# Performance work log

Hardware: AMD Instinct MI355X
Metric: run time of the kernel (lower is better)

Reference implementation:

```python
import jax, jax.numpy as jnp
import numpy as np

E = 32      # particle_embed_dim = q/k/v head out dim
G = 2       # nof_net_types (conv groups)
NEG_SLOPE = 0.01


def _glin(x, w, b, groups):
    """Grouped 1x1 conv on (M, C, 1, 1) == grouped linear.
    x: (M, Cin), w: (Cout, Cin//groups), b: (Cout,)."""
    M = x.shape[0]
    Cout = w.shape[0]
    xg = x.reshape(M, groups, -1)                 # (M, G, Cin/G)
    wg = w.reshape(groups, Cout // groups, -1)    # (G, Cout/G, Cin/G)
    y = jnp.einsum('mgi,goi->mgo', xg, wg).reshape(M, Cout)
    return y + b


def setup_inputs() -> dict:
    key = jax.random.key(0)
    ks = jax.random.split(key, 9)
    B, N = 32, 1024
    s = 0.05
    return {
        'x_e':   jax.random.normal(ks[0], (B, N, G * E), dtype=jnp.float32),
        'w_qkv': jax.random.normal(ks[1], (3 * G * E, E), dtype=jnp.float32) * s,
        'b_qkv': jax.random.normal(ks[2], (3 * G * E,), dtype=jnp.float32) * s,
        'w_h1':  jax.random.normal(ks[3], (G * E, 2 * E), dtype=jnp.float32) * s,
        'b_h1':  jax.random.normal(ks[4], (G * E,), dtype=jnp.float32) * s,
        'w_h10': jax.random.normal(ks[5], (G * E, E), dtype=jnp.float32) * s,
        'b_h10': jax.random.normal(ks[6], (G * E,), dtype=jnp.float32) * s,
        'w_h11': jax.random.normal(ks[7], (G * E, E), dtype=jnp.float32) * s,
        'b_h11': jax.random.normal(ks[8], (G * E,), dtype=jnp.float32) * s,
    }


def reference(x_e, w_qkv, b_qkv, w_h1, b_h1, w_h10, b_h10, w_h11, b_h11):
    B, N, D = x_e.shape                      # D = G*E = 64
    act = lambda z: jnp.where(z >= 0, z, NEG_SLOPE * z)

    # grouped 1x1-conv QKV projection
    qkv = _glin(x_e.reshape(B * N, D), w_qkv, b_qkv, G)        # (B*N, 3*G*E)
    qkv = qkv.reshape(B, N, G, 3, E).transpose(0, 2, 3, 1, 4)  # (B, G, 3, N, E)
    q, k, v = qkv[:, :, 0], qkv[:, :, 1], qkv[:, :, 2]         # each (B, G, N, E)

    # NOTE: module divides k by sqrt(E) and logits by sqrt(E) again -> 1/E total
    scale = 1.0 / E
    ip = jnp.einsum('bgne,bgme->bgnm', q, k) * scale           # (B, G, N, N)
    sip = jax.nn.softmax(ip, axis=-1)
    attn = jnp.einsum('bgnm,bgme->bgne', sip, v)               # (B, G, N, E)

    # concat pre-attention v with attention output, regroup per-particle
    x_xe = jnp.concatenate([v, attn], axis=3)                  # (B, G, N, 2E)
    x_xe = x_xe.transpose(0, 2, 1, 3).reshape(B * N, G * 2 * E)  # (B*N, 128)

    h = act(_glin(x_xe, w_h1, b_h1, G))
    h = act(_glin(h, w_h10, b_h10, G))
    h = act(_glin(h, w_h11, b_h11, G))
    return h.reshape(B * N, G * E, 1, 1)
```

## Files before the change

kernel.cpp:

```cpp
#include <hip/hip_runtime.h>

#define B_ 32
#define N_ 1024
#define G_ 2
#define E_ 32
#define M_ (B_*N_)
#define NEG 0.01f
#define QT 128
#define KT 128
#define QSC (1.4426950408889634f/32.0f)

using half8  = __attribute__((ext_vector_type(8))) _Float16;
using half4  = __attribute__((ext_vector_type(4))) _Float16;
using floatx4 = __attribute__((ext_vector_type(4))) float;

#if defined(__has_builtin)
#if __has_builtin(__builtin_amdgcn_exp2f)
#define EXP2(x) __builtin_amdgcn_exp2f(x)
#endif
#endif
#ifndef EXP2
#define EXP2(x) exp2f(x)
#endif

__global__ __launch_bounds__(256) void qkv_kernel(
    const float* __restrict__ x, const float* __restrict__ w, const float* __restrict__ bias,
    _Float16* __restrict__ Qh, _Float16* __restrict__ Kh,
    _Float16* __restrict__ Vh, _Float16* __restrict__ Vth)
{
    __shared__ _Float16 wsh[192*36];
    __shared__ float bsh[192];
    int t = threadIdx.x;
    for (int idx = t; idx < 192*32; idx += 256) {
        int r = idx >> 5, c = idx & 31;
        wsh[r*36 + c] = (_Float16)w[idx];
    }
    if (t < 192) bsh[t] = bias[t];
    __syncthreads();

    int lane = t & 63, wv = t >> 6;
    int L15 = lane & 15, quad = lane >> 4;
    int row0 = blockIdx.x*64 + wv*16;
    int b = row0 >> 10, nn0 = row0 & 1023;

    half4 ax[2][2];
    #pragma unroll
    for (int g2 = 0; g2 < 2; g2++)
        #pragma unroll
        for (int kt = 0; kt < 2; kt++) {
            float4 f = *(const float4*)(x + (size_t)(row0+L15)*64 + g2*32 + kt*16 + quad*4);
            half4 h = { (_Float16)f.x, (_Float16)f.y, (_Float16)f.z, (_Float16)f.w };
            ax[g2][kt] = h;
        }

    floatx4 acc[12];
    #pragma unroll
    for (int i = 0; i < 12; i++) acc[i] = (floatx4){0.f,0.f,0.f,0.f};

    #pragma unroll
    for (int g2 = 0; g2 < 2; g2++)
        #pragma unroll
        for (int nt = 0; nt < 6; nt++)
            #pragma unroll
            for (int kt = 0; kt < 2; kt++) {
                half4 bw = *(const half4*)&wsh[(g2*96+nt*16+L15)*36 + kt*16 + quad*4];
                acc[g2*6+nt] = __builtin_amdgcn_mfma_f32_16x16x16f16(ax[g2][kt], bw, acc[g2*6+nt], 0,0,0);
            }

    #pragma unroll
    for (int g2 = 0; g2 < 2; g2++) {
        size_t bg = (size_t)(b*2 + g2);
        #pragma unroll
        for (int nt = 0; nt < 6; nt++) {
            float bia = bsh[g2*96 + nt*16 + L15];
            floatx4 a4 = acc[g2*6+nt];
            int e = (nt & 1)*16 + L15;
            int kind = nt >> 1;
            if (kind == 0) {
                #pragma unroll
                for (int r = 0; r < 4; r++) {
                    int nn = nn0 + quad*4 + r;
                    Qh[(bg*N_ + nn)*32 + e] = (_Float16)((a4[r] + bia)*QSC);
                }
            } else if (kind == 1) {
                #pragma unroll
                for (int r = 0; r < 4; r++) {
                    int nn = nn0 + quad*4 + r;
                    Kh[(bg*N_ + nn)*32 + e] = (_Float16)(a4[r] + bia);
                }
            } else {
                half4 vv;
                #pragma unroll
                for (int r = 0; r < 4; r++) {
                    int nn = nn0 + quad*4 + r;
                    float vval = a4[r] + bia;
                    Vh[(bg*N_ + nn)*32 + e] = (_Float16)vval;
                    vv[r] = (_Float16)vval;
                }
                *(half4*)(Vth + (bg*32 + e)*N_ + nn0 + quad*4) = vv;
            }
        }
    }
}

struct __align__(16) SmemU {
    union {
        struct { _Float16 Kst[128*40]; _Float16 Vtst[32*136]; } a;
        _Float16 xs[128*72];
    } u;
    float linv[128];
    float bl1[32], bl10[32], bl11[32];
};

__global__ __launch_bounds__(256) void attn_mlp_kernel(
    const _Float16* __restrict__ Qh, const _Float16* __restrict__ Kh,
    const _Float16* __restrict__ Vh, const _Float16* __restrict__ Vth,
    const float* __restrict__ w_h1,  const float* __restrict__ b_h1,
    const float* __restrict__ w_h10, const float* __restrict__ b_h10,
    const float* __restrict__ w_h11, const float* __restrict__ b_h11,
    float* __restrict__ out)
{
    __shared__ SmemU sm;
    int t = threadIdx.x;
    int bg = blockIdx.x >> 3;
    int qtile = blockIdx.x & 7;
    int b = bg >> 1, g = bg & 1;
    int qbase = qtile * QT;
    size_t bgN = (size_t)bg * N_;

    if (t < 32) {
        sm.bl1[t]  = b_h1[g*32+t];
        sm.bl10[t] = b_h10[g*32+t];
        sm.bl11[t] = b_h11[g*32+t];
    }

    int lane = t & 63;
    int w    = t >> 6;
    int L15  = lane & 15;
    int quad = lane >> 4;
    int q0w  = qbase + w*32;

    half8 bq0 = *(const half8*)(Qh + (bgN + q0w +      L15)*32 + quad*8);
    half8 bq1 = *(const half8*)(Qh + (bgN + q0w + 16 + L15)*32 + quad*8);

    floatx4 o00 = {0.f,0.f,0.f,0.f}, o01 = o00, o10 = o00, o11 = o00;
    float lsum0 = 0.f, lsum1 = 0.f;

    for (int kt = 0; kt < N_/KT; kt++) {
        __syncthreads();
        #pragma unroll
        for (int it = 0; it < 2; it++) {
            int idx = t + it*256;
            int row = idx >> 2, c = idx & 3;
            half8 kv = *(const half8*)(Kh + (bgN + (size_t)kt*KT + row)*32 + c*8);
            *(half8*)&sm.u.a.Kst[row*40 + c*8] = kv;
        }
        #pragma unroll
        for (int it = 0; it < 2; it++) {
            int idx = t + it*256;
            int ee = idx >> 4, c = idx & 15;
            half8 vv = *(const half8*)(Vth + (size_t)bg*(32*N_) + (size_t)ee*N_ + kt*KT + c*8);
            *(half8*)&sm.u.a.Vtst[ee*136 + c*8] = vv;
        }
        __syncthreads();

        #pragma unroll
        for (int mt = 0; mt < 8; mt++) {
            half8 ak = *(const half8*)&sm.u.a.Kst[(mt*16 + L15)*40 + quad*8];
            floatx4 z = {0.f,0.f,0.f,0.f};
            floatx4 s0 = __builtin_amdgcn_mfma_f32_16x16x32_f16(ak, bq0, z, 0, 0, 0);
            floatx4 s1 = __builtin_amdgcn_mfma_f32_16x16x32_f16(ak, bq1, z, 0, 0, 0);
            float p00 = EXP2(s0.x), p01 = EXP2(s0.y), p02 = EXP2(s0.z), p03 = EXP2(s0.w);
            float p10 = EXP2(s1.x), p11 = EXP2(s1.y), p12 = EXP2(s1.z), p13 = EXP2(s1.w);
            lsum0 += (p00+p01)+(p02+p03);
            lsum1 += (p10+p11)+(p12+p13);
            half4 a0 = { (_Float16)p00, (_Float16)p01, (_Float16)p02, (_Float16)p03 };
            half4 a1 = { (_Float16)p10, (_Float16)p11, (_Float16)p12, (_Float16)p13 };
            half4 bv0 = *(const half4*)&sm.u.a.Vtst[      L15*136 + mt*16 + quad*4];
            half4 bv1 = *(const half4*)&sm.u.a.Vtst[(16+L15)*136 + mt*16 + quad*4];
            o00 = __builtin_amdgcn_mfma_f32_16x16x16f16(a0, bv0, o00, 0, 0, 0);
            o01 = __builtin_amdgcn_mfma_f32_16x16x16f16(a0, bv1, o01, 0, 0, 0);
            o10 = __builtin_amdgcn_mfma_f32_16x16x16f16(a1, bv0, o10, 0, 0, 0);
            o11 = __builtin_amdgcn_mfma_f32_16x16x16f16(a1, bv1, o11, 0, 0, 0);
        }
    }

    lsum0 += __shfl_xor(lsum0, 16, 64); lsum0 += __shfl_xor(lsum0, 32, 64);
    lsum1 += __shfl_xor(lsum1, 16, 64); lsum1 += __shfl_xor(lsum1, 32, 64);
    if (quad == 0) {
        sm.linv[w*32 +      L15] = 1.0f / lsum0;
        sm.linv[w*32 + 16 + L15] = 1.0f / lsum1;
    }
    __syncthreads();

    for (int idx = t; idx < 512; idx += 256) {
        int row = idx >> 2, c = idx & 3;
        half8 vv = *(const half8*)(Vh + (bgN + qbase + row)*32 + c*8);
        *(half8*)&sm.u.xs[row*72 + c*8] = vv;
    }
    {
        const floatx4* ofr[2][2] = { {&o00,&o01}, {&o10,&o11} };
        #pragma unroll
        for (int nt = 0; nt < 2; nt++) {
            float4 li = *(const float4*)&sm.linv[w*32 + nt*16 + quad*4];
            #pragma unroll
            for (int et = 0; et < 2; et++) {
                floatx4 ov = *ofr[nt][et];
                sm.u.xs[(w*32+nt*16+quad*4+0)*72 + 32 + et*16 + L15] = (_Float16)(ov[0]*li.x);
                sm.u.xs[(w*32+nt*16+quad*4+1)*72 + 32 + et*16 + L15] = (_Float16)(ov[1]*li.y);
                sm.u.xs[(w*32+nt*16+quad*4+2)*72 + 32 + et*16 + L15] = (_Float16)(ov[2]*li.z);
                sm.u.xs[(w*32+nt*16+quad*4+3)*72 + 32 + et*16 + L15] = (_Float16)(ov[3]*li.w);
            }
        }
    }
    __syncthreads();

    half4 a1f[2][4], a2f[2][2], a3f[2][2];
    #pragma unroll
    for (int mt = 0; mt < 2; mt++) {
        #pragma unroll
        for (int kt = 0; kt < 4; kt++) {
            float4 f = *(const float4*)(w_h1 + (size_t)(g*32+mt*16+L15)*64 + kt*16 + quad*4);
            half4 h = { (_Float16)f.x, (_Float16)f.y, (_Float16)f.z, (_Float16)f.w };
            a1f[mt][kt] = h;
        }
        #pragma unroll
        for (int kt = 0; kt < 2; kt++) {
            float4 f = *(const float4*)(w_h10 + (size_t)(g*32+mt*16+L15)*32 + kt*16 + quad*4);
            half4 h = { (_Float16)f.x, (_Float16)f.y, (_Float16)f.z, (_Float16)f.w };
            a2f[mt][kt] = h;
            float4 f2 = *(const float4*)(w_h11 + (size_t)(g*32+mt*16+L15)*32 + kt*16 + quad*4);
            half4 h2 = { (_Float16)f2.x, (_Float16)f2.y, (_Float16)f2.z, (_Float16)f2.w };
            a3f[mt][kt] = h2;
        }
    }

    floatx4 d1[2][2];
    #pragma unroll
    for (int mt = 0; mt < 2; mt++)
        #pragma unroll
        for (int nt = 0; nt < 2; nt++) d1[mt][nt] = (floatx4){0.f,0.f,0.f,0.f};
    #pragma unroll
    for (int nt = 0; nt < 2; nt++)
        #pragma unroll
        for (int kt = 0; kt < 4; kt++) {
            half4 b1 = *(const half4*)&sm.u.xs[(w*32+nt*16+L15)*72 + kt*16 + quad*4];
            d1[0][nt] = __builtin_amdgcn_mfma_f32_16x16x16f16(a1f[0][kt], b1, d1[0][nt], 0,0,0);
            d1[1][nt] = __builtin_amdgcn_mfma_f32_16x16x16f16(a1f[1][kt], b1, d1[1][nt], 0,0,0);
        }
    half4 h1b[2][2];
    #pragma unroll
    for (int mt = 0; mt < 2; mt++) {
        float4 bb = *(const float4*)&sm.bl1[mt*16 + quad*4];
        #pragma unroll
        for (int nt = 0; nt < 2; nt++) {
            float v0 = d1[mt][nt][0] + bb.x; v0 = (v0>=0.f)?v0:NEG*v0;
            float v1 = d1[mt][nt][1] + bb.y; v1 = (v1>=0.f)?v1:NEG*v1;
            float v2 = d1[mt][nt][2] + bb.z; v2 = (v2>=0.f)?v2:NEG*v2;
            float v3 = d1[mt][nt][3] + bb.w; v3 = (v3>=0.f)?v3:NEG*v3;
            half4 h = { (_Float16)v0, (_Float16)v1, (_Float16)v2, (_Float16)v3 };
            h1b[mt][nt] = h;
        }
    }
    floatx4 d2[2][2];
    #pragma unroll
    for (int mt = 0; mt < 2; mt++)
        #pragma unroll
        for (int nt = 0; nt < 2; nt++) d2[mt][nt] = (floatx4){0.f,0.f,0.f,0.f};
    #pragma unroll
    for (int mt = 0; mt < 2; mt++)
        #pragma unroll
        for (int nt = 0; nt < 2; nt++)
            #pragma unroll
            for (int kt = 0; kt < 2; kt++)
                d2[mt][nt] = __builtin_amdgcn_mfma_f32_16x16x16f16(a2f[mt][kt], h1b[kt][nt], d2[mt][nt], 0,0,0);
    half4 h2b[2][2];
    #pragma unroll
    for (int mt = 0; mt < 2; mt++) {
        float4 bb = *(const float4*)&sm.bl10[mt*16 + quad*4];
        #pragma unroll
        for (int nt = 0; nt < 2; nt++) {
            float v0 = d2[mt][nt][0] + bb.x; v0 = (v0>=0.f)?v0:NEG*v0;
            float v1 = d2[mt][nt][1] + bb.y; v1 = (v1>=0.f)?v1:NEG*v1;
            float v2 = d2[mt][nt][2] + bb.z; v2 = (v2>=0.f)?v2:NEG*v2;
            float v3 = d2[mt][nt][3] + bb.w; v3 = (v3>=0.f)?v3:NEG*v3;
            half4 h = { (_Float16)v0, (_Float16)v1, (_Float16)v2, (_Float16)v3 };
            h2b[mt][nt] = h;
        }
    }
    floatx4 d3[2][2];
    #pragma unroll
    for (int mt = 0; mt < 2; mt++)
        #pragma unroll
        for (int nt = 0; nt < 2; nt++) d3[mt][nt] = (floatx4){0.f,0.f,0.f,0.f};
    #pragma unroll
    for (int mt = 0; mt < 2; mt++)
        #pragma unroll
        for (int nt = 0; nt < 2; nt++)
            #pragma unroll
            for (int kt = 0; kt < 2; kt++)
                d3[mt][nt] = __builtin_amdgcn_mfma_f32_16x16x16f16(a3f[mt][kt], h2b[kt][nt], d3[mt][nt], 0,0,0);
    #pragma unroll
    for (int mt = 0; mt < 2; mt++) {
        float4 bb = *(const float4*)&sm.bl11[mt*16 + quad*4];
        #pragma unroll
        for (int nt = 0; nt < 2; nt++) {
            size_t rowbase = ((size_t)b*N_ + qbase + w*32 + nt*16 + L15)*64 + g*32 + mt*16 + quad*4;
            float v0 = d3[mt][nt][0] + bb.x; out[rowbase+0] = (v0>=0.f)?v0:NEG*v0;
            float v1 = d3[mt][nt][1] + bb.y; out[rowbase+1] = (v1>=0.f)?v1:NEG*v1;
            float v2 = d3[mt][nt][2] + bb.z; out[rowbase+2] = (v2>=0.f)?v2:NEG*v2;
            float v3 = d3[mt][nt][3] + bb.w; out[rowbase+3] = (v3>=0.f)?v3:NEG*v3;
        }
    }
}

extern "C" void kernel_launch(void* const* d_in, const int* in_sizes, int n_in,
                              void* d_out, int out_size, void* d_ws, size_t ws_size,
                              hipStream_t stream) {
    const float* x_e   = (const float*)d_in[0];
    const float* w_qkv = (const float*)d_in[1];
    const float* b_qkv = (const float*)d_in[2];
    const float* w_h1  = (const float*)d_in[3];
    const float* b_h1  = (const float*)d_in[4];
    const float* w_h10 = (const float*)d_in[5];
    const float* b_h10 = (const float*)d_in[6];
    const float* w_h11 = (const float*)d_in[7];
    const float* b_h11 = (const float*)d_in[8];
    float* out = (float*)d_out;

    const size_t qkv_elems = (size_t)B_*G_*N_*E_;
    _Float16* Qh  = (_Float16*)d_ws;
    _Float16* Kh  = Qh + qkv_elems;
    _Float16* Vh  = Kh + qkv_elems;
    _Float16* Vth = Vh + qkv_elems;

    hipLaunchKernelGGL(qkv_kernel, dim3(M_/64), dim3(256), 0, stream,
                       x_e, w_qkv, b_qkv, Qh, Kh, Vh, Vth);
    hipLaunchKernelGGL(attn_mlp_kernel, dim3(B_*G_*(N_/QT)), dim3(256), 0, stream,
                       Qh, Kh, Vh, Vth, w_h1, b_h1, w_h10, b_h10, w_h11, b_h11, out);
}
```

Measured before the change: 105.7 us.

## Halve attention query tile, stage QKV outputs in LDS for coalesced stores

The attention kernel now handles 64 queries per block with 16 per wave, doubling the grid to 1024 blocks and declaring 4 blocks per CU in the launch bounds for better occupancy. The QKV projection now writes Q, K, V and the transposed V into shared-memory tiles and then stores them to global memory as coalesced half8 vectors, replacing scattered 2-byte stores. The final MLP output is written as float4. In exchange, each block re-reads the full K and V^T for only 64 queries, doubling K/V traffic from L2, and the QKV kernel now uses more LDS.

After: 110.6 us. 1.05x slower.

```diff
diff --git a/kernel.cpp b/kernel.cpp
--- a/kernel.cpp
+++ b/kernel.cpp
@@ -6,7 +6,7 @@
 #define E_ 32
 #define M_ (B_*N_)
 #define NEG 0.01f
-#define QT 128
+#define QT 64
 #define KT 128
 #define QSC (1.4426950408889634f/32.0f)
 
@@ -30,6 +30,8 @@
 {
     __shared__ _Float16 wsh[192*36];
     __shared__ float bsh[192];
+    __shared__ _Float16 sQ[64*72], sK[64*72], sV[64*72];
+    __shared__ _Float16 vT[64*72];
     int t = threadIdx.x;
     for (int idx = t; idx < 192*32; idx += 256) {
         int r = idx >> 5, c = idx & 31;
@@ -41,7 +43,7 @@
     int lane = t & 63, wv = t >> 6;
     int L15 = lane & 15, quad = lane >> 4;
     int row0 = blockIdx.x*64 + wv*16;
-    int b = row0 >> 10, nn0 = row0 & 1023;
+    int b = row0 >> 10, nn0g = (blockIdx.x*64) & 1023;
 
     half4 ax[2][2];
     #pragma unroll
@@ -69,50 +71,61 @@
 
     #pragma unroll
     for (int g2 = 0; g2 < 2; g2++) {
-        size_t bg = (size_t)(b*2 + g2);
         #pragma unroll
         for (int nt = 0; nt < 6; nt++) {
             float bia = bsh[g2*96 + nt*16 + L15];
             floatx4 a4 = acc[g2*6+nt];
             int e = (nt & 1)*16 + L15;
             int kind = nt >> 1;
+            int rbase = wv*16 + quad*4;
             if (kind == 0) {
                 #pragma unroll
-                for (int r = 0; r < 4; r++) {
-                    int nn = nn0 + quad*4 + r;
-                    Qh[(bg*N_ + nn)*32 + e] = (_Float16)((a4[r] + bia)*QSC);
-                }
+                for (int r = 0; r < 4; r++)
+                    sQ[(rbase+r)*72 + g2*32 + e] = (_Float16)((a4[r] + bia)*QSC);
             } else if (kind == 1) {
                 #pragma unroll
-                for (int r = 0; r < 4; r++) {
-                    int nn = nn0 + quad*4 + r;
-                    Kh[(bg*N_ + nn)*32 + e] = (_Float16)(a4[r] + bia);
-                }
+                for (int r = 0; r < 4; r++)
+                    sK[(rbase+r)*72 + g2*32 + e] = (_Float16)(a4[r] + bia);
             } else {
                 half4 vv;
                 #pragma unroll
                 for (int r = 0; r < 4; r++) {
-                    int nn = nn0 + quad*4 + r;
                     float vval = a4[r] + bia;
-                    Vh[(bg*N_ + nn)*32 + e] = (_Float16)vval;
+                    sV[(rbase+r)*72 + g2*32 + e] = (_Float16)vval;
                     vv[r] = (_Float16)vval;
                 }
-                *(half4*)(Vth + (bg*32 + e)*N_ + nn0 + quad*4) = vv;
+                *(half4*)&vT[(g2*32+e)*72 + rbase] = vv;
             }
         }
+    }
+    __syncthreads();
+
+    int r = t >> 2, c8 = t & 3;
+    #pragma unroll
+    for (int g2 = 0; g2 < 2; g2++) {
+        size_t gbase = (((size_t)(b*2+g2))*N_ + nn0g + r)*32 + c8*8;
+        *(half8*)(Qh + gbase) = *(const half8*)&sQ[r*72 + g2*32 + c8*8];
+        *(half8*)(Kh + gbase) = *(const half8*)&sK[r*72 + g2*32 + c8*8];
+        *(half8*)(Vh + gbase) = *(const half8*)&sV[r*72 + g2*32 + c8*8];
+    }
+    #pragma unroll
+    for (int it = 0; it < 2; it++) {
+        int idx = t + it*256;
+        int ge = idx >> 3, c = idx & 7;
+        *(half8*)(Vth + ((size_t)(b*2)*32 + ge)*N_ + nn0g + c*8) = *(const half8*)&vT[ge*72 + c*8];
     }
 }
 
 struct __align__(16) SmemU {
     union {
         struct { _Float16 Kst[128*40]; _Float16 Vtst[32*136]; } a;
-        _Float16 xs[128*72];
+        _Float16 xs[64*72];
     } u;
-    float linv[128];
+    float linv[64];
     float bl1[32], bl10[32], bl11[32];
 };
 
-__global__ __launch_bounds__(256) void attn_mlp_kernel(
+__global__ __launch_bounds__(256, 4) void attn_mlp_kernel(
     const _Float16* __restrict__ Qh, const _Float16* __restrict__ Kh,
     const _Float16* __restrict__ Vh, const _Float16* __restrict__ Vth,
     const float* __restrict__ w_h1,  const float* __restrict__ b_h1,
@@ -122,8 +135,8 @@
 {
     __shared__ SmemU sm;
     int t = threadIdx.x;
-    int bg = blockIdx.x >> 3;
-    int qtile = blockIdx.x & 7;
+    int bg = blockIdx.x >> 4;
+    int qtile = blockIdx.x & 15;
     int b = bg >> 1, g = bg & 1;
     int qbase = qtile * QT;
     size_t bgN = (size_t)bg * N_;
@@ -138,13 +151,12 @@
     int w    = t >> 6;
     int L15  = lane & 15;
     int quad = lane >> 4;
-    int q0w  = qbase + w*32;
-
-    half8 bq0 = *(const half8*)(Qh + (bgN + q0w +      L15)*32 + quad*8);
-    half8 bq1 = *(const half8*)(Qh + (bgN + q0w + 16 + L15)*32 + quad*8);
-
-    floatx4 o00 = {0.f,0.f,0.f,0.f}, o01 = o00, o10 = o00, o11 = o00;
-    float lsum0 = 0.f, lsum1 = 0.f;
+    int q0w  = qbase + w*16;
+
+    half8 bq = *(const half8*)(Qh + (bgN + q0w + L15)*32 + quad*8);
+
+    floatx4 o0 = {0.f,0.f,0.f,0.f}, o1 = o0;
+    float lsum = 0.f;
 
     for (int kt = 0; kt < N_/KT; kt++) {
         __syncthreads();
@@ -168,49 +180,36 @@
         for (int mt = 0; mt < 8; mt++) {
             half8 ak = *(const half8*)&sm.u.a.Kst[(mt*16 + L15)*40 + quad*8];
             floatx4 z = {0.f,0.f,0.f,0.f};
-            floatx4 s0 = __builtin_amdgcn_mfma_f32_16x16x32_f16(ak, bq0, z, 0, 0, 0);
-            floatx4 s1 = __builtin_amdgcn_mfma_f32_16x16x32_f16(ak, bq1, z, 0, 0, 0);
-            float p00 = EXP2(s0.x), p01 = EXP2(s0.y), p02 = EXP2(s0.z), p03 = EXP2(s0.w);
-            float p10 = EXP2(s1.x), p11 = EXP2(s1.y), p12 = EXP2(s1.z), p13 = EXP2(s1.w);
-            lsum0 += (p00+p01)+(p02+p03);
-            lsum1 += (p10+p11)+(p12+p13);
-            half4 a0 = { (_Float16)p00, (_Float16)p01, (_Float16)p02, (_Float16)p03 };
-            half4 a1 = { (_Float16)p10, (_Float16)p11, (_Float16)p12, (_Float16)p13 };
+            floatx4 s = __builtin_amdgcn_mfma_f32_16x16x32_f16(ak, bq, z, 0, 0, 0);
+            float p0 = EXP2(s.x), p1 = EXP2(s.y), p2 = EXP2(s.z), p3 = EXP2(s.w);
+            lsum += (p0+p1)+(p2+p3);
+            half4 a0 = { (_Float16)p0, (_Float16)p1, (_Float16)p2, (_Float16)p3 };
             half4 bv0 = *(const half4*)&sm.u.a.Vtst[      L15*136 + mt*16 + quad*4];
             half4 bv1 = *(const half4*)&sm.u.a.Vtst[(16+L15)*136 + mt*16 + quad*4];
-            o00 = __builtin_amdgcn_mfma_f32_16x16x16f16(a0, bv0, o00, 0, 0, 0);
-            o01 = __builtin_amdgcn_mfma_f32_16x16x16f16(a0, bv1, o01, 0, 0, 0);
-            o10 = __builtin_amdgcn_mfma_f32_16x16x16f16(a1, bv0, o10, 0, 0, 0);
-            o11 = __builtin_amdgcn_mfma_f32_16x16x16f16(a1, bv1, o11, 0, 0, 0);
-        }
-    }
-
-    lsum0 += __shfl_xor(lsum0, 16, 64); lsum0 += __shfl_xor(lsum0, 32, 64);
-    lsum1 += __shfl_xor(lsum1, 16, 64); lsum1 += __shfl_xor(lsum1, 32, 64);
-    if (quad == 0) {
-        sm.linv[w*32 +      L15] = 1.0f / lsum0;
-        sm.linv[w*32 + 16 + L15] = 1.0f / lsum1;
-    }
+            o0 = __builtin_amdgcn_mfma_f32_16x16x16f16(a0, bv0, o0, 0, 0, 0);
+            o1 = __builtin_amdgcn_mfma_f32_16x16x16f16(a0, bv1, o1, 0, 0, 0);
+        }
+    }
+
+    lsum += __shfl_xor(lsum, 16, 64); lsum += __shfl_xor(lsum, 32, 64);
+    if (quad == 0) sm.linv[w*16 + L15] = 1.0f / lsum;
     __syncthreads();
 
-    for (int idx = t; idx < 512; idx += 256) {
-        int row = idx >> 2, c = idx & 3;
+    {
+        int row = t >> 2, c = t & 3;
         half8 vv = *(const half8*)(Vh + (bgN + qbase + row)*32 + c*8);
         *(half8*)&sm.u.xs[row*72 + c*8] = vv;
     }
     {
-        const floatx4* ofr[2][2] = { {&o00,&o01}, {&o10,&o11} };
-        #pragma unroll
-        for (int nt = 0; nt < 2; nt++) {
-            float4 li = *(const float4*)&sm.linv[w*32 + nt*16 + quad*4];
-            #pragma unroll
-            for (int et = 0; et < 2; et++) {
-                floatx4 ov = *ofr[nt][et];
-                sm.u.xs[(w*32+nt*16+quad*4+0)*72 + 32 + et*16 + L15] = (_Float16)(ov[0]*li.x);
-                sm.u.xs[(w*32+nt*16+quad*4+1)*72 + 32 + et*16 + L15] = (_Float16)(ov[1]*li.y);
-                sm.u.xs[(w*32+nt*16+quad*4+2)*72 + 32 + et*16 + L15] = (_Float16)(ov[2]*li.z);
-                sm.u.xs[(w*32+nt*16+quad*4+3)*72 + 32 + et*16 + L15] = (_Float16)(ov[3]*li.w);
-            }
+        float4 li = *(const float4*)&sm.linv[w*16 + quad*4];
+        const floatx4* ofr[2] = { &o0, &o1 };
+        #pragma unroll
+        for (int et = 0; et < 2; et++) {
+            floatx4 ov = *ofr[et];
+            sm.u.xs[(w*16+quad*4+0)*72 + 32 + et*16 + L15] = (_Float16)(ov[0]*li.x);
+            sm.u.xs[(w*16+quad*4+1)*72 + 32 + et*16 + L15] = (_Float16)(ov[1]*li.y);
+            sm.u.xs[(w*16+quad*4+2)*72 + 32 + et*16 + L15] = (_Float16)(ov[2]*li.z);
+            sm.u.xs[(w*16+quad*4+3)*72 + 32 + et*16 + L15] = (_Float16)(ov[3]*li.w);
         }
     }
     __syncthreads();
@@ -235,82 +234,56 @@
         }
     }
 
-    floatx4 d1[2][2];
-    #pragma unroll
-    for (int mt = 0; mt < 2; mt++)
-        #pragma unroll
-        for (int nt = 0; nt < 2; nt++) d1[mt][nt] = (floatx4){0.f,0.f,0.f,0.f};
-    #pragma unroll
-    for (int nt = 0; nt < 2; nt++)
-        #pragma unroll
-        for (int kt = 0; kt < 4; kt++) {
-            half4 b1 = *(const half4*)&sm.u.xs[(w*32+nt*16+L15)*72 + kt*16 + quad*4];
-            d1[0][nt] = __builtin_amdgcn_mfma_f32_16x16x16f16(a1f[0][kt], b1, d1[0][nt], 0,0,0);
-            d1[1][nt] = __builtin_amdgcn_mfma_f32_16x16x16f16(a1f[1][kt], b1, d1[1][nt], 0,0,0);
-        }
-    half4 h1b[2][2];
+    floatx4 d1[2] = { {0.f,0.f,0.f,0.f}, {0.f,0.f,0.f,0.f} };
+    #pragma unroll
+    for (int kt = 0; kt < 4; kt++) {
+        half4 b1 = *(const half4*)&sm.u.xs[(w*16+L15)*72 + kt*16 + quad*4];
+        d1[0] = __builtin_amdgcn_mfma_f32_16x16x16f16(a1f[0][kt], b1, d1[0], 0,0,0);
+        d1[1] = __builtin_amdgcn_mfma_f32_16x16x16f16(a1f[1][kt], b1, d1[1], 0,0,0);
+    }
+    half4 h1b[2];
     #pragma unroll
     for (int mt = 0; mt < 2; mt++) {
         float4 bb = *(const float4*)&sm.bl1[mt*16 + quad*4];
-        #pragma unroll
-        for (int nt = 0; nt < 2; nt++) {
-            float v0 = d1[mt][nt][0] + bb.x; v0 = (v0>=0.f)?v0:NEG*v0;
-            float v1 = d1[mt][nt][1] + bb.y; v1 = (v1>=0.f)?v1:NEG*v1;
-            float v2 = d1[mt][nt][2] + bb.z; v2 = (v2>=0.f)?v2:NEG*v2;
-            float v3 = d1[mt][nt][3] + bb.w; v3 = (v3>=0.f)?v3:NEG*v3;
-            half4 h = { (_Float16)v0, (_Float16)v1, (_Float16)v2, (_Float16)v3 };
-            h1b[mt][nt] = h;
-        }
-    }
-    floatx4 d2[2][2];
+        float v0 = d1[mt][0] + bb.x; v0 = (v0>=0.f)?v0:NEG*v0;
+        float v1 = d1[mt][1] + bb.y; v1 = (v1>=0.f)?v1:NEG*v1;
+        float v2 = d1[mt][2] + bb.z; v2 = (v2>=0.f)?v2:NEG*v2;
+        float v3 = d1[mt][3] + bb.w; v3 = (v3>=0.f)?v3:NEG*v3;
+        half4 h = { (_Float16)v0, (_Float16)v1, (_Float16)v2, (_Float16)v3 };
+        h1b[mt] = h;
+    }
+    floatx4 d2[2] = { {0.f,0.f,0.f,0.f}, {0.f,0.f,0.f,0.f} };
     #pragma unroll
     for (int mt = 0; mt < 2; mt++)
         #pragma unroll
-        for (int nt = 0; nt < 2; nt++) d2[mt][nt] = (floatx4){0.f,0.f,0.f,0.f};
-    #pragma unroll
-    for (int mt = 0; mt < 2; mt++)
-        #pragma unroll
-        for (int nt = 0; nt < 2; nt++)
-            #pragma unroll
-            for (int kt = 0; kt < 2; kt++)
-                d2[mt][nt] = __builtin_amdgcn_mfma_f32_16x16x16f16(a2f[mt][kt], h1b[kt][nt], d2[mt][nt], 0,0,0);
-    half4 h2b[2][2];
+        for (int kt = 0; kt < 2; kt++)
+            d2[mt] = __builtin_amdgcn_mfma_f32_16x16x16f16(a2f[mt][kt], h1b[kt], d2[mt], 0,0,0);
+    half4 h2b[2];
     #pragma unroll
     for (int mt = 0; mt < 2; mt++) {
         float4 bb = *(const float4*)&sm.bl10[mt*16 + quad*4];
-        #pragma unroll
-        for (int nt = 0; nt < 2; nt++) {
-            float v0 = d2[mt][nt][0] + bb.x; v0 = (v0>=0.f)?v0:NEG*v0;
-            float v1 = d2[mt][nt][1] + bb.y; v1 = (v1>=0.f)?v1:NEG*v1;
-            float v2 = d2[mt][nt][2] + bb.z; v2 = (v2>=0.f)?v2:NEG*v2;
-            float v3 = d2[mt][nt][3] + bb.w; v3 = (v3>=0.f)?v3:NEG*v3;
-            half4 h = { (_Float16)v0, (_Float16)v1, (_Float16)v2, (_Float16)v3 };
-            h2b[mt][nt] = h;
-        }
-    }
-    floatx4 d3[2][2];
+        float v0 = d2[mt][0] + bb.x; v0 = (v0>=0.f)?v0:NEG*v0;
+        float v1 = d2[mt][1] + bb.y; v1 = (v1>=0.f)?v1:NEG*v1;
+        float v2 = d2[mt][2] + bb.z; v2 = (v2>=0.f)?v2:NEG*v2;
+        float v3 = d2[mt][3] + bb.w; v3 = (v3>=0.f)?v3:NEG*v3;
+        half4 h = { (_Float16)v0, (_Float16)v1, (_Float16)v2, (_Float16)v3 };
+        h2b[mt] = h;
+    }
+    floatx4 d3[2] = { {0.f,0.f,0.f,0.f}, {0.f,0.f,0.f,0.f} };
     #pragma unroll
     for (int mt = 0; mt < 2; mt++)
         #pragma unroll
-        for (int nt = 0; nt < 2; nt++) d3[mt][nt] = (floatx4){0.f,0.f,0.f,0.f};
-    #pragma unroll
-    for (int mt = 0; mt < 2; mt++)
-        #pragma unroll
-        for (int nt = 0; nt < 2; nt++)
-            #pragma unroll
-            for (int kt = 0; kt < 2; kt++)
-                d3[mt][nt] = __builtin_amdgcn_mfma_f32_16x16x16f16(a3f[mt][kt], h2b[kt][nt], d3[mt][nt], 0,0,0);
+        for (int kt = 0; kt < 2; kt++)
+            d3[mt] = __builtin_amdgcn_mfma_f32_16x16x16f16(a3f[mt][kt], h2b[kt], d3[mt], 0,0,0);
     #pragma unroll
     for (int mt = 0; mt < 2; mt++) {
         float4 bb = *(const float4*)&sm.bl11[mt*16 + quad*4];
-        #pragma unroll
-        for (int nt = 0; nt < 2; nt++) {
-            size_t rowbase = ((size_t)b*N_ + qbase + w*32 + nt*16 + L15)*64 + g*32 + mt*16 + quad*4;
-            float v0 = d3[mt][nt][0] + bb.x; out[rowbase+0] = (v0>=0.f)?v0:NEG*v0;
-            float v1 = d3[mt][nt][1] + bb.y; out[rowbase+1] = (v1>=0.f)?v1:NEG*v1;
-            float v2 = d3[mt][nt][2] + bb.z; out[rowbase+2] = (v2>=0.f)?v2:NEG*v2;
-            float v3 = d3[mt][nt][3] + bb.w; out[rowbase+3] = (v3>=0.f)?v3:NEG*v3;
-        }
+        float4 ov;
+        ov.x = d3[mt][0] + bb.x; ov.x = (ov.x>=0.f)?ov.x:NEG*ov.x;
+        ov.y = d3[mt][1] + bb.y; ov.y = (ov.y>=0.f)?ov.y:NEG*ov.y;
+        ov.z = d3[mt][2] + bb.z; ov.z = (ov.z>=0.f)?ov.z:NEG*ov.z;
+        ov.w = d3[mt][3] + bb.w; ov.w = (ov.w>=0.f)?ov.w:NEG*ov.w;
+        *(float4*)(out + ((size_t)b*N_ + qbase + w*16 + L15)*64 + g*32 + mt*16 + quad*4) = ov;
     }
 }
 
```

## Fuse QKV projection into attention kernel, recomputing K/V per query tile

Applied to the files above, without the earlier changes.

Removes the separate QKV kernel and its fp16 Q/K/V/Vt workspace round-trip. Each attention block now computes its own Q tile and recomputes K and V for every key tile straight from x with MFMA, prefetching the next x tile from global memory. This trades redundant projection work (K/V recomputed 8 times per batch-group) for one fewer launch and less global traffic. The output stores are also vectorised to float4, and launch bounds now request 2 blocks per SM.

Result: faster. 100.1 us (-5.3%).

```diff
diff --git a/kernel.cpp b/kernel.cpp
--- a/kernel.cpp
+++ b/kernel.cpp
@@ -2,12 +2,7 @@
 
 #define B_ 32
 #define N_ 1024
-#define G_ 2
-#define E_ 32
-#define M_ (B_*N_)
 #define NEG 0.01f
-#define QT 128
-#define KT 128
 #define QSC (1.4426950408889634f/32.0f)
 
 using half8  = __attribute__((ext_vector_type(8))) _Float16;
@@ -23,165 +18,160 @@
 #define EXP2(x) exp2f(x)
 #endif
 
-__global__ __launch_bounds__(256) void qkv_kernel(
-    const float* __restrict__ x, const float* __restrict__ w, const float* __restrict__ bias,
-    _Float16* __restrict__ Qh, _Float16* __restrict__ Kh,
-    _Float16* __restrict__ Vh, _Float16* __restrict__ Vth)
-{
-    __shared__ _Float16 wsh[192*36];
-    __shared__ float bsh[192];
-    int t = threadIdx.x;
-    for (int idx = t; idx < 192*32; idx += 256) {
-        int r = idx >> 5, c = idx & 31;
-        wsh[r*36 + c] = (_Float16)w[idx];
-    }
-    if (t < 192) bsh[t] = bias[t];
-    __syncthreads();
-
-    int lane = t & 63, wv = t >> 6;
-    int L15 = lane & 15, quad = lane >> 4;
-    int row0 = blockIdx.x*64 + wv*16;
-    int b = row0 >> 10, nn0 = row0 & 1023;
-
-    half4 ax[2][2];
-    #pragma unroll
-    for (int g2 = 0; g2 < 2; g2++)
-        #pragma unroll
-        for (int kt = 0; kt < 2; kt++) {
-            float4 f = *(const float4*)(x + (size_t)(row0+L15)*64 + g2*32 + kt*16 + quad*4);
-            half4 h = { (_Float16)f.x, (_Float16)f.y, (_Float16)f.z, (_Float16)f.w };
-            ax[g2][kt] = h;
-        }
-
-    floatx4 acc[12];
-    #pragma unroll
-    for (int i = 0; i < 12; i++) acc[i] = (floatx4){0.f,0.f,0.f,0.f};
-
-    #pragma unroll
-    for (int g2 = 0; g2 < 2; g2++)
-        #pragma unroll
-        for (int nt = 0; nt < 6; nt++)
-            #pragma unroll
-            for (int kt = 0; kt < 2; kt++) {
-                half4 bw = *(const half4*)&wsh[(g2*96+nt*16+L15)*36 + kt*16 + quad*4];
-                acc[g2*6+nt] = __builtin_amdgcn_mfma_f32_16x16x16f16(ax[g2][kt], bw, acc[g2*6+nt], 0,0,0);
-            }
-
-    #pragma unroll
-    for (int g2 = 0; g2 < 2; g2++) {
-        size_t bg = (size_t)(b*2 + g2);
-        #pragma unroll
-        for (int nt = 0; nt < 6; nt++) {
-            float bia = bsh[g2*96 + nt*16 + L15];
-            floatx4 a4 = acc[g2*6+nt];
-            int e = (nt & 1)*16 + L15;
-            int kind = nt >> 1;
-            if (kind == 0) {
-                #pragma unroll
-                for (int r = 0; r < 4; r++) {
-                    int nn = nn0 + quad*4 + r;
-                    Qh[(bg*N_ + nn)*32 + e] = (_Float16)((a4[r] + bia)*QSC);
-                }
-            } else if (kind == 1) {
-                #pragma unroll
-                for (int r = 0; r < 4; r++) {
-                    int nn = nn0 + quad*4 + r;
-                    Kh[(bg*N_ + nn)*32 + e] = (_Float16)(a4[r] + bia);
-                }
-            } else {
-                half4 vv;
-                #pragma unroll
-                for (int r = 0; r < 4; r++) {
-                    int nn = nn0 + quad*4 + r;
-                    float vval = a4[r] + bia;
-                    Vh[(bg*N_ + nn)*32 + e] = (_Float16)vval;
-                    vv[r] = (_Float16)vval;
-                }
-                *(half4*)(Vth + (bg*32 + e)*N_ + nn0 + quad*4) = vv;
-            }
-        }
-    }
+__device__ inline half8 cvt8(float4 a, float4 b) {
+    half8 h;
+    h[0]=(_Float16)a.x; h[1]=(_Float16)a.y; h[2]=(_Float16)a.z; h[3]=(_Float16)a.w;
+    h[4]=(_Float16)b.x; h[5]=(_Float16)b.y; h[6]=(_Float16)b.z; h[7]=(_Float16)b.w;
+    return h;
 }
 
-struct __align__(16) SmemU {
+struct __align__(16) Smem {
+    _Float16 wsh[96*36];
+    float    bsh[96];
+    _Float16 Kst[128*40];
+    _Float16 Vtst[32*136];
     union {
-        struct { _Float16 Kst[128*40]; _Float16 Vtst[32*136]; } a;
+        _Float16 qs[128*40];
         _Float16 xs[128*72];
     } u;
     float linv[128];
     float bl1[32], bl10[32], bl11[32];
 };
 
-__global__ __launch_bounds__(256) void attn_mlp_kernel(
-    const _Float16* __restrict__ Qh, const _Float16* __restrict__ Kh,
-    const _Float16* __restrict__ Vh, const _Float16* __restrict__ Vth,
+__global__ __launch_bounds__(256, 2) void fused_kernel(
+    const float* __restrict__ x, const float* __restrict__ w_qkv, const float* __restrict__ b_qkv,
     const float* __restrict__ w_h1,  const float* __restrict__ b_h1,
     const float* __restrict__ w_h10, const float* __restrict__ b_h10,
     const float* __restrict__ w_h11, const float* __restrict__ b_h11,
     float* __restrict__ out)
 {
-    __shared__ SmemU sm;
+    __shared__ Smem sm;
     int t = threadIdx.x;
     int bg = blockIdx.x >> 3;
     int qtile = blockIdx.x & 7;
     int b = bg >> 1, g = bg & 1;
-    int qbase = qtile * QT;
-    size_t bgN = (size_t)bg * N_;
-
+    int qbase = qtile * 128;
+    int lane = t & 63, w = t >> 6;
+    int L15 = lane & 15, quad = lane >> 4;
+
+    for (int idx = t; idx < 96*32; idx += 256) {
+        int r = idx >> 5, c = idx & 31;
+        sm.wsh[r*36 + c] = (_Float16)w_qkv[(g*96 + r)*32 + c];
+    }
+    if (t < 96) sm.bsh[t] = b_qkv[g*96 + t];
     if (t < 32) {
         sm.bl1[t]  = b_h1[g*32+t];
         sm.bl10[t] = b_h10[g*32+t];
         sm.bl11[t] = b_h11[g*32+t];
     }
-
-    int lane = t & 63;
-    int w    = t >> 6;
-    int L15  = lane & 15;
-    int quad = lane >> 4;
-    int q0w  = qbase + w*32;
-
-    half8 bq0 = *(const half8*)(Qh + (bgN + q0w +      L15)*32 + quad*8);
-    half8 bq1 = *(const half8*)(Qh + (bgN + q0w + 16 + L15)*32 + quad*8);
+    __syncthreads();
+
+    half8 bwq[2], bwk[2], bwv[2];
+    float bqv[2], bkv[2], bvv[2];
+    #pragma unroll
+    for (int et = 0; et < 2; et++) {
+        bwq[et] = *(const half8*)&sm.wsh[(     et*16 + L15)*36 + quad*8];
+        bwk[et] = *(const half8*)&sm.wsh[(32 + et*16 + L15)*36 + quad*8];
+        bwv[et] = *(const half8*)&sm.wsh[(64 + et*16 + L15)*36 + quad*8];
+        bqv[et] = sm.bsh[     et*16 + L15];
+        bkv[et] = sm.bsh[32 + et*16 + L15];
+        bvv[et] = sm.bsh[64 + et*16 + L15];
+    }
+
+    {
+        floatx4 z = {0.f,0.f,0.f,0.f};
+        floatx4 dq[2][2];
+        #pragma unroll
+        for (int mt = 0; mt < 2; mt++) {
+            const float* p = x + ((size_t)b*N_ + qbase + w*32 + mt*16 + L15)*64 + g*32 + quad*8;
+            float4 f0 = *(const float4*)p;
+            float4 f1 = *(const float4*)(p + 4);
+            half8 axq = cvt8(f0, f1);
+            dq[mt][0] = __builtin_amdgcn_mfma_f32_16x16x32_f16(axq, bwq[0], z, 0,0,0);
+            dq[mt][1] = __builtin_amdgcn_mfma_f32_16x16x32_f16(axq, bwq[1], z, 0,0,0);
+        }
+        #pragma unroll
+        for (int mt = 0; mt < 2; mt++)
+            #pragma unroll
+            for (int et = 0; et < 2; et++)
+                #pragma unroll
+                for (int r = 0; r < 4; r++)
+                    sm.u.qs[(w*32 + mt*16 + quad*4 + r)*40 + et*16 + L15] =
+                        (_Float16)((dq[mt][et][r] + bqv[et])*QSC);
+    }
+    __syncthreads();
+    half8 bq0 = *(const half8*)&sm.u.qs[(w*32 +      L15)*40 + quad*8];
+    half8 bq1 = *(const half8*)&sm.u.qs[(w*32 + 16 + L15)*40 + quad*8];
+
+    float4 xf0[2], xf1[2];
+    #pragma unroll
+    for (int mt = 0; mt < 2; mt++) {
+        const float* p = x + ((size_t)b*N_ + 0*128 + w*32 + mt*16 + L15)*64 + g*32 + quad*8;
+        xf0[mt] = *(const float4*)p;
+        xf1[mt] = *(const float4*)(p + 4);
+    }
 
     floatx4 o00 = {0.f,0.f,0.f,0.f}, o01 = o00, o10 = o00, o11 = o00;
     float lsum0 = 0.f, lsum1 = 0.f;
 
-    for (int kt = 0; kt < N_/KT; kt++) {
+    for (int kt = 0; kt < 8; kt++) {
+        floatx4 z = {0.f,0.f,0.f,0.f};
+        floatx4 dK[2][2], dV[2][2];
+        #pragma unroll
+        for (int mt = 0; mt < 2; mt++) {
+            half8 axk = cvt8(xf0[mt], xf1[mt]);
+            dK[mt][0] = __builtin_amdgcn_mfma_f32_16x16x32_f16(axk, bwk[0], z, 0,0,0);
+            dK[mt][1] = __builtin_amdgcn_mfma_f32_16x16x32_f16(axk, bwk[1], z, 0,0,0);
+            dV[mt][0] = __builtin_amdgcn_mfma_f32_16x16x32_f16(axk, bwv[0], z, 0,0,0);
+            dV[mt][1] = __builtin_amdgcn_mfma_f32_16x16x32_f16(axk, bwv[1], z, 0,0,0);
+        }
         __syncthreads();
         #pragma unroll
-        for (int it = 0; it < 2; it++) {
-            int idx = t + it*256;
-            int row = idx >> 2, c = idx & 3;
-            half8 kv = *(const half8*)(Kh + (bgN + (size_t)kt*KT + row)*32 + c*8);
-            *(half8*)&sm.u.a.Kst[row*40 + c*8] = kv;
-        }
-        #pragma unroll
-        for (int it = 0; it < 2; it++) {
-            int idx = t + it*256;
-            int ee = idx >> 4, c = idx & 15;
-            half8 vv = *(const half8*)(Vth + (size_t)bg*(32*N_) + (size_t)ee*N_ + kt*KT + c*8);
-            *(half8*)&sm.u.a.Vtst[ee*136 + c*8] = vv;
+        for (int mt = 0; mt < 2; mt++) {
+            int rb = w*32 + mt*16 + quad*4;
+            #pragma unroll
+            for (int et = 0; et < 2; et++) {
+                half4 vh;
+                #pragma unroll
+                for (int r = 0; r < 4; r++) {
+                    sm.Kst[(rb + r)*40 + et*16 + L15] = (_Float16)(dK[mt][et][r] + bkv[et]);
+                    vh[r] = (_Float16)(dV[mt][et][r] + bvv[et]);
+                }
+                *(half4*)&sm.Vtst[(et*16 + L15)*136 + rb] = vh;
+                if (kt == qtile) {
+                    #pragma unroll
+                    for (int r = 0; r < 4; r++)
+                        sm.u.xs[(rb + r)*72 + et*16 + L15] = vh[r];
+                }
+            }
         }
         __syncthreads();
-
-        #pragma unroll
-        for (int mt = 0; mt < 8; mt++) {
-            half8 ak = *(const half8*)&sm.u.a.Kst[(mt*16 + L15)*40 + quad*8];
-            floatx4 z = {0.f,0.f,0.f,0.f};
-            floatx4 s0 = __builtin_amdgcn_mfma_f32_16x16x32_f16(ak, bq0, z, 0, 0, 0);
-            floatx4 s1 = __builtin_amdgcn_mfma_f32_16x16x32_f16(ak, bq1, z, 0, 0, 0);
+        if (kt < 7) {
+            #pragma unroll
+            for (int mt = 0; mt < 2; mt++) {
+                const float* p = x + ((size_t)b*N_ + (kt+1)*128 + w*32 + mt*16 + L15)*64 + g*32 + quad*8;
+                xf0[mt] = *(const float4*)p;
+                xf1[mt] = *(const float4*)(p + 4);
+            }
+        }
+        #pragma unroll
+        for (int mt8 = 0; mt8 < 8; mt8++) {
+            half8 ak = *(const half8*)&sm.Kst[(mt8*16 + L15)*40 + quad*8];
+            floatx4 zz = {0.f,0.f,0.f,0.f};
+            floatx4 s0 = __builtin_amdgcn_mfma_f32_16x16x32_f16(ak, bq0, zz, 0,0,0);
+            floatx4 s1 = __builtin_amdgcn_mfma_f32_16x16x32_f16(ak, bq1, zz, 0,0,0);
             float p00 = EXP2(s0.x), p01 = EXP2(s0.y), p02 = EXP2(s0.z), p03 = EXP2(s0.w);
             float p10 = EXP2(s1.x), p11 = EXP2(s1.y), p12 = EXP2(s1.z), p13 = EXP2(s1.w);
             lsum0 += (p00+p01)+(p02+p03);
             lsum1 += (p10+p11)+(p12+p13);
             half4 a0 = { (_Float16)p00, (_Float16)p01, (_Float16)p02, (_Float16)p03 };
             half4 a1 = { (_Float16)p10, (_Float16)p11, (_Float16)p12, (_Float16)p13 };
-            half4 bv0 = *(const half4*)&sm.u.a.Vtst[      L15*136 + mt*16 + quad*4];
-            half4 bv1 = *(const half4*)&sm.u.a.Vtst[(16+L15)*136 + mt*16 + quad*4];
-            o00 = __builtin_amdgcn_mfma_f32_16x16x16f16(a0, bv0, o00, 0, 0, 0);
-            o01 = __builtin_amdgcn_mfma_f32_16x16x16f16(a0, bv1, o01, 0, 0, 0);
-            o10 = __builtin_amdgcn_mfma_f32_16x16x16f16(a1, bv0, o10, 0, 0, 0);
-            o11 = __builtin_amdgcn_mfma_f32_16x16x16f16(a1, bv1, o11, 0, 0, 0);
+            half4 bv0 = *(const half4*)&sm.Vtst[      L15*136 + mt8*16 + quad*4];
+            half4 bv1 = *(const half4*)&sm.Vtst[(16 + L15)*136 + mt8*16 + quad*4];
+            o00 = __builtin_amdgcn_mfma_f32_16x16x16f16(a0, bv0, o00, 0,0,0);
+            o01 = __builtin_amdgcn_mfma_f32_16x16x16f16(a0, bv1, o01, 0,0,0);
+            o10 = __builtin_amdgcn_mfma_f32_16x16x16f16(a1, bv0, o10, 0,0,0);
+            o11 = __builtin_amdgcn_mfma_f32_16x16x16f16(a1, bv1, o11, 0,0,0);
         }
     }
 
@@ -193,11 +183,6 @@
     }
     __syncthreads();
 
-    for (int idx = t; idx < 512; idx += 256) {
-        int row = idx >> 2, c = idx & 3;
-        half8 vv = *(const half8*)(Vh + (bgN + qbase + row)*32 + c*8);
-        *(half8*)&sm.u.xs[row*72 + c*8] = vv;
-    }
     {
         const floatx4* ofr[2][2] = { {&o00,&o01}, {&o10,&o11} };
         #pragma unroll
@@ -305,11 +290,12 @@
         float4 bb = *(const float4*)&sm.bl11[mt*16 + quad*4];
         #pragma unroll
         for (int nt = 0; nt < 2; nt++) {
-            size_t rowbase = ((size_t)b*N_ + qbase + w*32 + nt*16 + L15)*64 + g*32 + mt*16 + quad*4;
-            float v0 = d3[mt][nt][0] + bb.x; out[rowbase+0] = (v0>=0.f)?v0:NEG*v0;
-            float v1 = d3[mt][nt][1] + bb.y; out[rowbase+1] = (v1>=0.f)?v1:NEG*v1;
-            float v2 = d3[mt][nt][2] + bb.z; out[rowbase+2] = (v2>=0.f)?v2:NEG*v2;
-            float v3 = d3[mt][nt][3] + bb.w; out[rowbase+3] = (v3>=0.f)?v3:NEG*v3;
+            float4 ov;
+            ov.x = d3[mt][nt][0] + bb.x; ov.x = (ov.x>=0.f)?ov.x:NEG*ov.x;
+            ov.y = d3[mt][nt][1] + bb.y; ov.y = (ov.y>=0.f)?ov.y:NEG*ov.y;
+            ov.z = d3[mt][nt][2] + bb.z; ov.z = (ov.z>=0.f)?ov.z:NEG*ov.z;
+            ov.w = d3[mt][nt][3] + bb.w; ov.w = (ov.w>=0.f)?ov.w:NEG*ov.w;
+            *(float4*)(out + ((size_t)b*N_ + qbase + w*32 + nt*16 + L15)*64 + g*32 + mt*16 + quad*4) = ov;
         }
     }
 }
@@ -328,14 +314,6 @@
     const float* b_h11 = (const float*)d_in[8];
     float* out = (float*)d_out;
 
-    const size_t qkv_elems = (size_t)B_*G_*N_*E_;
-    _Float16* Qh  = (_Float16*)d_ws;
-    _Float16* Kh  = Qh + qkv_elems;
-    _Float16* Vh  = Kh + qkv_elems;
-    _Float16* Vth = Vh + qkv_elems;
-
-    hipLaunchKernelGGL(qkv_kernel, dim3(M_/64), dim3(256), 0, stream,
-                       x_e, w_qkv, b_qkv, Qh, Kh, Vh, Vth);
-    hipLaunchKernelGGL(attn_mlp_kernel, dim3(B_*G_*(N_/QT)), dim3(256), 0, stream,
-                       Qh, Kh, Vh, Vth, w_h1, b_h1, w_h10, b_h10, w_h11, b_h11, out);
+    hipLaunchKernelGGL(fused_kernel, dim3(B_*2*8), dim3(256), 0, stream,
+                       x_e, w_qkv, b_qkv, w_h1, b_h1, w_h10, b_h10, w_h11, b_h11, out);
 }
```
